# Performance work log

Measured on AMD Instinct MI355X. Metric: run time of the kernel, lower is better.

## Reference

```python
import jax, jax.numpy as jnp
import numpy as np

H = 8  # num_heads


def _ln(x, g, b):
    mu = x.mean(-1, keepdims=True)
    var = ((x - mu) ** 2).mean(-1, keepdims=True)
    return (x - mu) * jax.lax.rsqrt(var + 1e-5) * g + b


def setup_inputs() -> dict:
    key = jax.random.key(0)
    ks = jax.random.split(key, 24)
    B, N, V, E, D, R, L = 8, 512, 50000, 300, 256, 100, 4
    dh = D // H
    s = 0.02
    inp = {}
    inp['token_ids'] = jax.random.randint(ks[0], (B, N), 0, V, dtype=jnp.int32)
    inp['relations'] = jax.random.randint(ks[1], (B, N, N), 0, R, dtype=jnp.int32)
    m = jax.random.bernoulli(ks[2], 0.9, (B, N, N))
    eye = jnp.eye(N, dtype=bool)[None]
    inp['relations_mask'] = jnp.logical_or(m, eye)  # keep diagonal valid so every row attends somewhere
    inp['embed'] = jax.random.normal(ks[3], (V, E), jnp.float32) * s
    inp['W_in'] = jax.random.normal(ks[4], (E, D), jnp.float32) * s
    inp['b_in'] = jnp.zeros((D,), jnp.float32)
    inp['Wq'] = jax.random.normal(ks[5], (L, D, D), jnp.float32) * s
    inp['Wk'] = jax.random.normal(ks[6], (L, D, D), jnp.float32) * s
    inp['Wv'] = jax.random.normal(ks[7], (L, D, D), jnp.float32) * s
    inp['Wo'] = jax.random.normal(ks[8], (L, D, D), jnp.float32) * s
    inp['ln1_g'] = jnp.ones((L, D), jnp.float32)
    inp['ln1_b'] = jnp.zeros((L, D), jnp.float32)
    inp['ln2_g'] = jnp.ones((L, D), jnp.float32)
    inp['ln2_b'] = jnp.zeros((L, D), jnp.float32)
    inp['W1'] = jax.random.normal(ks[9], (L, D, 4 * D), jnp.float32) * s
    inp['b1'] = jnp.zeros((L, 4 * D), jnp.float32)
    inp['W2'] = jax.random.normal(ks[10], (L, 4 * D, D), jnp.float32) * s
    inp['b2'] = jnp.zeros((L, D), jnp.float32)
    inp['rel_k_emb'] = jax.random.normal(ks[11], (R, dh), jnp.float32) * s
    inp['rel_v_emb'] = jax.random.normal(ks[12], (R, dh), jnp.float32) * s
    inp['W_out'] = jax.random.normal(ks[13], (D, D), jnp.float32) * s
    inp['b_out'] = jnp.zeros((D,), jnp.float32)
    return inp


def reference(token_ids, relations, relations_mask, embed, W_in, b_in, Wq, Wk, Wv, Wo,
              ln1_g, ln1_b, ln2_g, ln2_b, W1, b1, W2, b2, rel_k_emb, rel_v_emb, W_out, b_out):
    # Input layer: embedding lookup + projection to gnn hidden size.
    x = embed[token_ids]                          # [B,N,E]
    x = jax.nn.relu(x @ W_in + b_in)              # [B,N,D]
    B, N, D = x.shape
    dh = D // H
    # Shared relation embeddings (share_layers=True, share_heads=True): gathered once.
    rk = rel_k_emb[relations]                     # [B,N,N,dh]
    rv = rel_v_emb[relations]                     # [B,N,N,dh]
    neg = jnp.asarray(-1e9, x.dtype)
    scale = jnp.asarray(1.0 / np.sqrt(dh), x.dtype)
    L = Wq.shape[0]
    for l in range(L):  # fixed small layer count
        q = (x @ Wq[l]).reshape(B, N, H, dh).transpose(0, 2, 1, 3)
        k = (x @ Wk[l]).reshape(B, N, H, dh).transpose(0, 2, 1, 3)
        v = (x @ Wv[l]).reshape(B, N, H, dh).transpose(0, 2, 1, 3)
        # Relation-aware scores: q.k + q.r_k (RAT-SQL)
        scores = (jnp.einsum('bhnd,bhmd->bhnm', q, k)
                  + jnp.einsum('bhnd,bnmd->bhnm', q, rk)) * scale
        scores = jnp.where(relations_mask[:, None], scores, neg)
        a = jax.nn.softmax(scores, axis=-1)       # [B,H,N,N]
        z = (jnp.einsum('bhnm,bhmd->bhnd', a, v)
             + jnp.einsum('bhnm,bnmd->bhnd', a, rv))
        z = z.transpose(0, 2, 1, 3).reshape(B, N, D) @ Wo[l]
        x = _ln(x + z, ln1_g[l], ln1_b[l])
        f = jax.nn.relu(x @ W1[l] + b1[l]) @ W2[l] + b2[l]
        x = _ln(x + f, ln2_g[l], ln2_b[l])
    # Output layer projection
    return x @ W_out + b_out
```

## Files before the change

### kernel.cpp

```cpp
#include <hip/hip_runtime.h>
#include <hip/hip_bf16.h>

#define NTOK 4096
#define NN   512

typedef __attribute__((ext_vector_type(8))) short bf16x8;
typedef __attribute__((ext_vector_type(4))) short bf16x4;
typedef __attribute__((ext_vector_type(4))) float f32x4;

__device__ __forceinline__ float bf16_to_f(unsigned short u) {
    unsigned int x = ((unsigned int)u) << 16;
    return __builtin_bit_cast(float, x);
}
__device__ __forceinline__ unsigned short f_to_bf16(float f) {
    unsigned int b = __builtin_bit_cast(unsigned int, f);
    return (unsigned short)((b + 0x7fff + ((b >> 16) & 1)) >> 16);
}
__device__ __forceinline__ bf16x8 pack8(float4 a, float4 b) {
    bf16x8 v;
    v[0]=(short)f_to_bf16(a.x); v[1]=(short)f_to_bf16(a.y);
    v[2]=(short)f_to_bf16(a.z); v[3]=(short)f_to_bf16(a.w);
    v[4]=(short)f_to_bf16(b.x); v[5]=(short)f_to_bf16(b.y);
    v[6]=(short)f_to_bf16(b.z); v[7]=(short)f_to_bf16(b.w);
    return v;
}

__global__ void detect_mask_kernel(const unsigned char* __restrict__ m, int* __restrict__ flag) {
    __shared__ int f;
    if (threadIdx.x == 0) f = 0;
    __syncthreads();
    int any = 0;
    for (int i = threadIdx.x; i < 4096; i += 256) {
        if ((i & 3) != 0 && m[i] != 0) any = 1;
    }
    if (any) atomicOr(&f, 1);
    __syncthreads();
    if (threadIdx.x == 0) *flag = f;
}

__global__ __launch_bounds__(256) void prep_rel16(
    const int* __restrict__ rel, const void* __restrict__ mask,
    const int* __restrict__ flag, short* __restrict__ rel16)
{
    const bool mbyte = (*flag != 0);
    const unsigned char* m8 = (const unsigned char*)mask;
    const int* m32 = (const int*)mask;
    const int i = (blockIdx.x * 256 + threadIdx.x) * 2;
    int2 rv = *(const int2*)(rel + i);
    int ok0, ok1;
    if (mbyte) { ok0 = m8[i]; ok1 = m8[i + 1]; }
    else       { ok0 = (m32[i] != 0); ok1 = (m32[i + 1] != 0); }
    short2 o;
    o.x = ok0 ? (short)rv.x : (short)-1;
    o.y = ok1 ? (short)rv.y : (short)-1;
    *(short2*)(rel16 + i) = o;
}

__global__ __launch_bounds__(256) void embed_proj_kernel(
    const int* __restrict__ tok, const float* __restrict__ embed,
    const float* __restrict__ W_in, const float* __restrict__ b_in,
    float* __restrict__ x)
{
    __shared__ float emb[8][304];
    __shared__ int tloc[8];
    const int t = threadIdx.x;
    const int r0 = blockIdx.x * 8;
    if (t < 8) tloc[t] = tok[r0 + t];
    __syncthreads();
    for (int i = t; i < 8 * 300; i += 256) {
        int r = i / 300, e = i - r * 300;
        emb[r][e] = embed[(size_t)tloc[r] * 300 + e];
    }
    __syncthreads();
    float acc[8] = {0.f,0.f,0.f,0.f,0.f,0.f,0.f,0.f};
    const int d = t;
    for (int e = 0; e < 300; ++e) {
        float w = W_in[e * 256 + d];
#pragma unroll
        for (int r = 0; r < 8; ++r) acc[r] += emb[r][e] * w;
    }
    const float bb = b_in[d];
#pragma unroll
    for (int r = 0; r < 8; ++r) {
        float o = acc[r] + bb;
        o = o > 0.f ? o : 0.f;
        x[(size_t)(r0 + r) * 256 + d] = o;
    }
}

__global__ __launch_bounds__(256) void gemm_mfma(
    const float* __restrict__ A,
    const float* __restrict__ W0, const float* __restrict__ W1p, const float* __restrict__ W2p,
    int ncPerW, const float* __restrict__ bias,
    float* __restrict__ C, int M, int K, int Nc, int relu)
{
    __shared__ unsigned short As[2][64][40];
    __shared__ unsigned short Bs[2][64][40];

    const int t = threadIdx.x;
    const int lane = t & 63, w = t >> 6;
    const int g = lane >> 4, li = lane & 15;
    const int r0 = blockIdx.y * 64, c0 = blockIdx.x * 64;

    const float* Wp = W0; int cW = c0;
    if (c0 >= 2 * ncPerW)      { Wp = W2p; cW = c0 - 2 * ncPerW; }
    else if (c0 >= ncPerW)     { Wp = W1p; cW = c0 - ncPerW; }

    f32x4 acc[4];
#pragma unroll
    for (int i = 0; i < 4; ++i) acc[i] = (f32x4){0.f, 0.f, 0.f, 0.f};

    const int arow = t >> 2, ad8 = (t & 3) * 8;
    const int bnn = t & 63, bk8 = (t >> 6) * 8;

    const float* ap0 = A + (size_t)(r0 + arow) * K + ad8;
    float4 a0 = *(const float4*)ap0;
    float4 a1 = *(const float4*)(ap0 + 4);
    float wv[8];
#pragma unroll
    for (int j = 0; j < 8; ++j)
        wv[j] = Wp[(size_t)(bk8 + j) * ncPerW + cW + bnn];

    const int nk = K >> 5;
    for (int ki = 0; ki < nk; ++ki) {
        const int cur = ki & 1;
        *(bf16x8*)&As[cur][arow][ad8] = pack8(a0, a1);
        {
            bf16x8 v;
#pragma unroll
            for (int j = 0; j < 8; ++j) v[j] = (short)f_to_bf16(wv[j]);
            *(bf16x8*)&Bs[cur][bnn][bk8] = v;
        }
        if (ki + 1 < nk) {
            const int k0 = (ki + 1) * 32;
            const float* ap = A + (size_t)(r0 + arow) * K + k0 + ad8;
            a0 = *(const float4*)ap;
            a1 = *(const float4*)(ap + 4);
#pragma unroll
            for (int j = 0; j < 8; ++j)
                wv[j] = Wp[(size_t)(k0 + bk8 + j) * ncPerW + cW + bnn];
        }
        __syncthreads();
        bf16x8 af = *(const bf16x8*)&As[cur][16 * w + li][g * 8];
#pragma unroll
        for (int sub = 0; sub < 4; ++sub) {
            bf16x8 bfr = *(const bf16x8*)&Bs[cur][16 * sub + li][g * 8];
            acc[sub] = __builtin_amdgcn_mfma_f32_16x16x32_bf16(af, bfr, acc[sub], 0, 0, 0);
        }
    }
#pragma unroll
    for (int sub = 0; sub < 4; ++sub) {
        int col = c0 + sub * 16 + li;
        float bv = bias ? bias[col] : 0.f;
#pragma unroll
        for (int r = 0; r < 4; ++r) {
            int row = r0 + 16 * w + g * 4 + r;
            float o = acc[sub][r] + bv;
            if (relu) o = fmaxf(o, 0.f);
            C[(size_t)row * Nc + col] = o;
        }
    }
}

__global__ __launch_bounds__(256) void gemm_mfma_128(
    const float* __restrict__ A,
    const float* __restrict__ W0, const float* __restrict__ W1p, const float* __restrict__ W2p,
    int ncPerW, const float* __restrict__ bias,
    float* __restrict__ C, int M, int K, int Nc, int relu)
{
    __shared__ unsigned short As[2][128][40];
    __shared__ unsigned short Bs[2][64][40];

    const int t = threadIdx.x;
    const int lane = t & 63, w = t >> 6;
    const int g = lane >> 4, li = lane & 15;
    const int r0 = blockIdx.y * 128, c0 = blockIdx.x * 64;

    const float* Wp = W0; int cW = c0;
    if (c0 >= 2 * ncPerW)      { Wp = W2p; cW = c0 - 2 * ncPerW; }
    else if (c0 >= ncPerW)     { Wp = W1p; cW = c0 - ncPerW; }

    f32x4 acc[2][4];
#pragma unroll
    for (int i = 0; i < 2; ++i)
#pragma unroll
        for (int j = 0; j < 4; ++j) acc[i][j] = (f32x4){0.f, 0.f, 0.f, 0.f};

    const int arow = t >> 1, ah = (t & 1) * 16;
    const int bnn = t & 63, bk8 = (t >> 6) * 8;

    const float* ap0 = A + (size_t)(r0 + arow) * K + ah;
    float4 a0 = *(const float4*)ap0;
    float4 a1 = *(const float4*)(ap0 + 4);
    float4 a2 = *(const float4*)(ap0 + 8);
    float4 a3 = *(const float4*)(ap0 + 12);
    float wv[8];
#pragma unroll
    for (int j = 0; j < 8; ++j)
        wv[j] = Wp[(size_t)(bk8 + j) * ncPerW + cW + bnn];

    const int nk = K >> 5;
    for (int ki = 0; ki < nk; ++ki) {
        const int cur = ki & 1;
        *(bf16x8*)&As[cur][arow][ah]     = pack8(a0, a1);
        *(bf16x8*)&As[cur][arow][ah + 8] = pack8(a2, a3);
        {
            bf16x8 v;
#pragma unroll
            for (int j = 0; j < 8; ++j) v[j] = (short)f_to_bf16(wv[j]);
            *(bf16x8*)&Bs[cur][bnn][bk8] = v;
        }
        if (ki + 1 < nk) {
            const int k0 = (ki + 1) * 32;
            const float* ap = A + (size_t)(r0 + arow) * K + k0 + ah;
            a0 = *(const float4*)ap;
            a1 = *(const float4*)(ap + 4);
            a2 = *(const float4*)(ap + 8);
            a3 = *(const float4*)(ap + 12);
#pragma unroll
            for (int j = 0; j < 8; ++j)
                wv[j] = Wp[(size_t)(k0 + bk8 + j) * ncPerW + cW + bnn];
        }
        __syncthreads();
        bf16x8 af0 = *(const bf16x8*)&As[cur][32 * w + li][g * 8];
        bf16x8 af1 = *(const bf16x8*)&As[cur][32 * w + 16 + li][g * 8];
#pragma unroll
        for (int sub = 0; sub < 4; ++sub) {
            bf16x8 bfr = *(const bf16x8*)&Bs[cur][16 * sub + li][g * 8];
            acc[0][sub] = __builtin_amdgcn_mfma_f32_16x16x32_bf16(af0, bfr, acc[0][sub], 0, 0, 0);
            acc[1][sub] = __builtin_amdgcn_mfma_f32_16x16x32_bf16(af1, bfr, acc[1][sub], 0, 0, 0);
        }
    }
#pragma unroll
    for (int rc = 0; rc < 2; ++rc)
#pragma unroll
    for (int sub = 0; sub < 4; ++sub) {
        int col = c0 + sub * 16 + li;
        float bv = bias ? bias[col] : 0.f;
#pragma unroll
        for (int r = 0; r < 4; ++r) {
            int row = r0 + 32 * w + rc * 16 + g * 4 + r;
            float o = acc[rc][sub][r] + bv;
            if (relu) o = fmaxf(o, 0.f);
            C[(size_t)row * Nc + col] = o;
        }
    }
}

__global__ __launch_bounds__(256) void qrk_kernel(
    const float* __restrict__ qkv, const float* __restrict__ relk_g,
    unsigned short* __restrict__ qrkg)
{
    const int n0 = blockIdx.x * 64, h = blockIdx.y, b = blockIdx.z;
    const int t = threadIdx.x, lane = t & 63, w = t >> 6;
    const int g = lane >> 4, li = lane & 15;
    const int qrow = 16 * w + g * 4;

    __shared__ unsigned short relk_s[100][40];
    for (int i = t; i < 400; i += 256) {
        int rr = i >> 2, d8 = (i & 3) * 8;
        const float* sp = relk_g + rr * 32 + d8;
        *(bf16x8*)&relk_s[rr][d8] = pack8(*(const float4*)sp, *(const float4*)(sp + 4));
    }
    const float scale = 0.17677669529663687f;
    bf16x8 qf;
    {
        const float* qp = qkv + (size_t)(b * NN + n0 + 16 * w + li) * 768 + h * 32 + g * 8;
        float4 q0 = *(const float4*)qp, q1 = *(const float4*)(qp + 4);
        q0.x *= scale; q0.y *= scale; q0.z *= scale; q0.w *= scale;
        q1.x *= scale; q1.y *= scale; q1.z *= scale; q1.w *= scale;
        qf = pack8(q0, q1);
    }
    __syncthreads();
#pragma unroll
    for (int rc = 0; rc < 7; ++rc) {
        bf16x8 bb = *(const bf16x8*)&relk_s[rc * 16 + li][g * 8];
        f32x4 s = __builtin_amdgcn_mfma_f32_16x16x32_bf16(qf, bb, (f32x4){0.f,0.f,0.f,0.f}, 0, 0, 0);
        int col = rc * 16 + li;
        if (col < 100) {
#pragma unroll
            for (int r = 0; r < 4; ++r)
                qrkg[((size_t)(b * 8 + h) * NN + n0 + qrow + r) * 100 + col] = f_to_bf16(s[r]);
        }
    }
}

__global__ __launch_bounds__(256, 4) void attn_mfma(
    const float* __restrict__ qkv,
    const short* __restrict__ rel16,
    const unsigned short* __restrict__ qrkg,
    const float* __restrict__ relv_g,
    float* __restrict__ zpart,
    float* __restrict__ smpart)
{
    const int p = blockIdx.x;
    const int cx = p & 7, idx0 = p >> 3;
    const int sg = cx * 8 + (idx0 >> 4);
    const int hm = idx0 & 15;
    const int h = hm >> 1, ms = hm & 1;
    const int b = sg >> 3, chunk = sg & 7;
    const int n0 = chunk * 64, mbase = ms * 256;

    const int t = threadIdx.x;
    const int lane = t & 63, w = t >> 6;
    const int g = lane >> 4, li = lane & 15;
    const int qrow = 16 * w + g * 4;

    __shared__ float wrel[64][100];
    __shared__ union {
        unsigned short relvT[32][136];
        struct {
            unsigned short v_t[2][32][40];
            unsigned short p_s[4][16][40];
        } mn;
    } u;

    for (int i = t; i < 6400; i += 256) ((float*)wrel)[i] = 0.f;
    const float scale = 0.17677669529663687f;
    bf16x8 qf;
    {
        const float* qp = qkv + (size_t)(b * NN + n0 + 16 * w + li) * 768 + h * 32 + g * 8;
        float4 q0 = *(const float4*)qp, q1 = *(const float4*)(qp + 4);
        q0.x *= scale; q0.y *= scale; q0.z *= scale; q0.w *= scale;
        q1.x *= scale; q1.y *= scale; q1.z *= scale; q1.w *= scale;
        qf = pack8(q0, q1);
    }
    const short* relrow[4];
    const unsigned short* qgr[4];
#pragma unroll
    for (int r = 0; r < 4; ++r) {
        relrow[r] = rel16 + ((size_t)b * NN + n0 + qrow + r) * NN;
        qgr[r] = qrkg + ((size_t)(b * 8 + h) * NN + n0 + qrow + r) * 100;
    }
    const int vm = t & 31, vdg = t >> 5;
    const size_t kRB = (size_t)(b * NN) * 768 + 256 + h * 32 + g * 8;
    const size_t vRB = (size_t)(b * NN) * 768 + 512 + h * 32 + vdg * 4;

    float4 kbuf[2][4]; float4 vbuf[2];
    short rbuf[2][8]; unsigned short qvb[2][8];
    {
#pragma unroll
        for (int i = 0; i < 8; ++i)
            rbuf[0][i] = relrow[i & 3][mbase + (i >> 2) * 16 + li];
        kbuf[0][0] = *(const float4*)(qkv + kRB + (size_t)(mbase + li) * 768);
        kbuf[0][1] = *(const float4*)(qkv + kRB + (size_t)(mbase + li) * 768 + 4);
        kbuf[0][2] = *(const float4*)(qkv + kRB + (size_t)(mbase + 16 + li) * 768);
        kbuf[0][3] = *(const float4*)(qkv + kRB + (size_t)(mbase + 16 + li) * 768 + 4);
        vbuf[0]    = *(const float4*)(qkv + vRB + (size_t)(mbase + vm) * 768);
#pragma unroll
        for (int i = 0; i < 8; ++i) {
            int rl = rbuf[0][i];
            qvb[0][i] = qgr[i & 3][rl < 0 ? 0 : rl];
        }
    }
    float smacc[4] = {0.f, 0.f, 0.f, 0.f};
    f32x4 zf[2];
    zf[0] = (f32x4){0.f,0.f,0.f,0.f};
    zf[1] = (f32x4){0.f,0.f,0.f,0.f};

    __syncthreads();

#pragma unroll
    for (int tt = 0; tt < 8; ++tt) {
        const int cur = tt & 1, nxt = cur ^ 1;
        {
            float4 vv = vbuf[cur];
            u.mn.v_t[cur][vdg * 4 + 0][vm] = f_to_bf16(vv.x);
            u.mn.v_t[cur][vdg * 4 + 1][vm] = f_to_bf16(vv.y);
            u.mn.v_t[cur][vdg * 4 + 2][vm] = f_to_bf16(vv.z);
            u.mn.v_t[cur][vdg * 4 + 3][vm] = f_to_bf16(vv.w);
        }
        if (tt + 1 < 8) {
            const int m0n = mbase + (tt + 1) * 32;
#pragma unroll
            for (int i = 0; i < 8; ++i)
                rbuf[nxt][i] = relrow[i & 3][m0n + (i >> 2) * 16 + li];
        }
        __syncthreads();
        bf16x8 kf0 = pack8(kbuf[cur][0], kbuf[cur][1]);
        bf16x8 kf1 = pack8(kbuf[cur][2], kbuf[cur][3]);
        if (tt + 1 < 8) {
            const int m0n = mbase + (tt + 1) * 32;
            kbuf[nxt][0] = *(const float4*)(qkv + kRB + (size_t)(m0n + li) * 768);
            kbuf[nxt][1] = *(const float4*)(qkv + kRB + (size_t)(m0n + li) * 768 + 4);
            kbuf[nxt][2] = *(const float4*)(qkv + kRB + (size_t)(m0n + 16 + li) * 768);
            kbuf[nxt][3] = *(const float4*)(qkv + kRB + (size_t)(m0n + 16 + li) * 768 + 4);
            vbuf[nxt]    = *(const float4*)(qkv + vRB + (size_t)(m0n + vm) * 768);
        }
        f32x4 s0 = __builtin_amdgcn_mfma_f32_16x16x32_bf16(qf, kf0, (f32x4){0.f,0.f,0.f,0.f}, 0, 0, 0);
        f32x4 s1 = __builtin_amdgcn_mfma_f32_16x16x32_bf16(qf, kf1, (f32x4){0.f,0.f,0.f,0.f}, 0, 0, 0);
        float pr[8];
#pragma unroll
        for (int i = 0; i < 8; ++i) {
            const int r = i & 3;
            const int rl = rbuf[cur][i];
            const float sv = ((i >> 2) ? s1[r] : s0[r]) + bf16_to_f(qvb[cur][i]);
            float pv = 0.f;
            if (rl >= 0) {
                pv = __expf(fminf(sv, 50.f));
                atomicAdd(&wrel[qrow + r][rl], pv);
            }
            smacc[r] += pv;
            pr[i] = pv;
        }
#pragma unroll
        for (int i = 0; i < 8; ++i)
            u.mn.p_s[w][g * 4 + (i & 3)][(i >> 2) * 16 + li] = f_to_bf16(pr[i]);
        if (tt + 1 < 8) {
#pragma unroll
            for (int i = 0; i < 8; ++i) {
                int rl = rbuf[nxt][i];
                qvb[nxt][i] = qgr[i & 3][rl < 0 ? 0 : rl];
            }
        }
        asm volatile("s_waitcnt lgkmcnt(0)" ::: "memory");
        __builtin_amdgcn_sched_barrier(0);
        bf16x8 pa = *(const bf16x8*)&u.mn.p_s[w][li][g * 8];
#pragma unroll
        for (int dc = 0; dc < 2; ++dc) {
            bf16x8 vb = *(const bf16x8*)&u.mn.v_t[cur][dc * 16 + li][g * 8];
            zf[dc] = __builtin_amdgcn_mfma_f32_16x16x32_bf16(pa, vb, zf[dc], 0, 0, 0);
        }
    }
    __syncthreads();

    for (int i = t; i < 32 * 36; i += 256) {
        int d = i / 36, c = 100 + (i - (i / 36) * 36);
        u.relvT[d][c] = 0;
    }
    for (int i = t; i < 400; i += 256) {
        int rr2 = i >> 2, d8 = (i & 3) * 8;
        const float* sp = relv_g + rr2 * 32 + d8;
        float4 s0 = *(const float4*)sp, s1 = *(const float4*)(sp + 4);
        u.relvT[d8 + 0][rr2] = f_to_bf16(s0.x);
        u.relvT[d8 + 1][rr2] = f_to_bf16(s0.y);
        u.relvT[d8 + 2][rr2] = f_to_bf16(s0.z);
        u.relvT[d8 + 3][rr2] = f_to_bf16(s0.w);
        u.relvT[d8 + 4][rr2] = f_to_bf16(s1.x);
        u.relvT[d8 + 5][rr2] = f_to_bf16(s1.y);
        u.relvT[d8 + 6][rr2] = f_to_bf16(s1.z);
        u.relvT[d8 + 7][rr2] = f_to_bf16(s1.w);
    }
    __syncthreads();

#pragma unroll
    for (int kc = 0; kc < 4; ++kc) {
        const int kbase = kc * 32 + g * 8;
        const float* wp = &wrel[16 * w + li][0];
        bf16x8 af;
#pragma unroll
        for (int j = 0; j < 8; ++j) {
            int id = kbase + j;
            float val = (id < 100) ? wp[id] : 0.f;
            af[j] = (short)f_to_bf16(val);
        }
#pragma unroll
        for (int dc = 0; dc < 2; ++dc) {
            bf16x8 vb = *(const bf16x8*)&u.relvT[dc * 16 + li][kbase];
            zf[dc] = __builtin_amdgcn_mfma_f32_16x16x32_bf16(af, vb, zf[dc], 0, 0, 0);
        }
    }

#pragma unroll
    for (int r = 0; r < 4; ++r) {
        smacc[r] += __shfl_xor(smacc[r], 1, 64);
        smacc[r] += __shfl_xor(smacc[r], 2, 64);
        smacc[r] += __shfl_xor(smacc[r], 4, 64);
        smacc[r] += __shfl_xor(smacc[r], 8, 64);
    }
#pragma unroll
    for (int r = 0; r < 4; ++r) {
        const int row = b * NN + n0 + qrow + r;
        size_t ob = (size_t)ms * 1048576 + (size_t)row * 256 + h * 32;
#pragma unroll
        for (int dc = 0; dc < 2; ++dc)
            zpart[ob + dc * 16 + li] = zf[dc][r];
        if (li == 0)
            smpart[(size_t)ms * 32768 + (size_t)row * 8 + h] = smacc[r];
    }
}

__global__ __launch_bounds__(256) void combine_kernel(
    const float* __restrict__ zpart, const float* __restrict__ smpart,
    float* __restrict__ z)
{
    const int t = threadIdx.x;
    const int wi = t >> 6, lane = t & 63;
    const int row = blockIdx.x * 4 + wi;
    const int h = lane >> 3;
    float den = 0.f;
    float4 acc = make_float4(0.f, 0.f, 0.f, 0.f);
#pragma unroll
    for (int s = 0; s < 2; ++s) {
        den += smpart[(size_t)s * 32768 + (size_t)row * 8 + h];
        float4 v = *(const float4*)(zpart + (size_t)s * 1048576 + (size_t)row * 256 + lane * 4);
        acc.x += v.x; acc.y += v.y; acc.z += v.z; acc.w += v.w;
    }
    const float inv = 1.f / den;
    acc.x *= inv; acc.y *= inv; acc.z *= inv; acc.w *= inv;
    *(float4*)(z + (size_t)row * 256 + lane * 4) = acc;
}

__global__ __launch_bounds__(256) void ln_kernel(
    const float* __restrict__ xin, const float* __restrict__ y,
    const float* __restrict__ g, const float* __restrict__ bsh,
    float* __restrict__ xout)
{
    const int t = threadIdx.x;
    const int w = t >> 6, lane = t & 63;
    const size_t row = (size_t)blockIdx.x * 4 + w;
    const float4 xv = *(const float4*)(xin + row * 256 + lane * 4);
    const float4 yv = *(const float4*)(y + row * 256 + lane * 4);
    float4 sv;
    sv.x = xv.x + yv.x; sv.y = xv.y + yv.y; sv.z = xv.z + yv.z; sv.w = xv.w + yv.w;
    float sum = sv.x + sv.y + sv.z + sv.w;
    float sq  = sv.x * sv.x + sv.y * sv.y + sv.z * sv.z + sv.w * sv.w;
#pragma unroll
    for (int off = 1; off < 64; off <<= 1) {
        sum += __shfl_xor(sum, off, 64);
        sq  += __shfl_xor(sq, off, 64);
    }
    const float mu = sum * (1.f / 256.f);
    const float var = sq * (1.f / 256.f) - mu * mu;
    const float rs = rsqrtf(var + 1e-5f);
    const float4 gv = *(const float4*)(g + lane * 4);
    const float4 bv = *(const float4*)(bsh + lane * 4);
    float4 o;
    o.x = (sv.x - mu) * rs * gv.x + bv.x;
    o.y = (sv.y - mu) * rs * gv.y + bv.y;
    o.z = (sv.z - mu) * rs * gv.z + bv.z;
    o.w = (sv.w - mu) * rs * gv.w + bv.w;
    *(float4*)(xout + row * 256 + lane * 4) = o;
}

extern "C" void kernel_launch(void* const* d_in, const int* in_sizes, int n_in,
                              void* d_out, int out_size, void* d_ws, size_t ws_size,
                              hipStream_t stream)
{
    (void)in_sizes; (void)n_in; (void)out_size;
    const int*   tok   = (const int*)d_in[0];
    const int*   rel   = (const int*)d_in[1];
    const void*  mask  = d_in[2];
    const float* embed = (const float*)d_in[3];
    const float* W_in  = (const float*)d_in[4];
    const float* b_in  = (const float*)d_in[5];
    const float* Wq    = (const float*)d_in[6];
    const float* Wk    = (const float*)d_in[7];
    const float* Wv    = (const float*)d_in[8];
    const float* Wo    = (const float*)d_in[9];
    const float* ln1g  = (const float*)d_in[10];
    const float* ln1b  = (const float*)d_in[11];
    const float* ln2g  = (const float*)d_in[12];
    const float* ln2b  = (const float*)d_in[13];
    const float* W1    = (const float*)d_in[14];
    const float* b1    = (const float*)d_in[15];
    const float* W2    = (const float*)d_in[16];
    const float* b2    = (const float*)d_in[17];
    const float* relk  = (const float*)d_in[18];
    const float* relv  = (const float*)d_in[19];
    const float* Wout  = (const float*)d_in[20];
    const float* bout  = (const float*)d_in[21];
    float* out = (float*)d_out;

    float* ws  = (float*)d_ws;
    float* x   = ws;
    float* z   = ws + (1u << 20);
    float* zo  = ws + 2u * (1u << 20);
    float* qkv = ws + 3u * (1u << 20);
    float* hb  = ws + 6u * (1u << 20);

    const bool roomy = ws_size >= ((size_t)45 << 20);
    short* rel16 = roomy ? (short*)(ws + 10u * (1u << 20)) : (short*)z;
    int*   flag  = (int*)(ws + (roomy ? 11u : 10u) * (1u << 20));
    float* zpart = hb;
    unsigned short* qrkg = (unsigned short*)(hb + 2u * (1u << 20));
    float* smpart = zo;

    detect_mask_kernel<<<1, 256, 0, stream>>>((const unsigned char*)mask, flag);
    if (roomy)
        prep_rel16<<<4096, 256, 0, stream>>>(rel, mask, flag, rel16);
    embed_proj_kernel<<<512, 256, 0, stream>>>(tok, embed, W_in, b_in, x);

    for (int l = 0; l < 4; ++l) {
        const float* wq = Wq + (size_t)l * 65536;
        const float* wk = Wk + (size_t)l * 65536;
        const float* wv = Wv + (size_t)l * 65536;
        const float* wo = Wo + (size_t)l * 65536;
        const float* w1 = W1 + (size_t)l * 262144;
        const float* w2 = W2 + (size_t)l * 262144;

        if (!roomy)
            prep_rel16<<<4096, 256, 0, stream>>>(rel, mask, flag, rel16);

        gemm_mfma_128<<<dim3(12, 32), 256, 0, stream>>>(x, wq, wk, wv, 256, nullptr,
                                                        qkv, NTOK, 256, 768, 0);
        qrk_kernel<<<dim3(8, 8, 8), 256, 0, stream>>>(qkv, relk, qrkg);
        attn_mfma<<<1024, 256, 0, stream>>>(qkv, rel16, qrkg, relv, zpart, smpart);
        combine_kernel<<<1024, 256, 0, stream>>>(zpart, smpart, z);
        gemm_mfma<<<dim3(4, 64), 256, 0, stream>>>(z, wo, wo, wo, 256, nullptr,
                                                   zo, NTOK, 256, 256, 0);
        ln_kernel<<<1024, 256, 0, stream>>>(x, zo, ln1g + l * 256, ln1b + l * 256, x);
        gemm_mfma_128<<<dim3(16, 32), 256, 0, stream>>>(x, w1, w1, w1, 1024, b1 + l * 1024,
                                                        hb, NTOK, 256, 1024, 1);
        gemm_mfma<<<dim3(4, 64), 256, 0, stream>>>(hb, w2, w2, w2, 256, b2 + l * 256,
                                                   zo, NTOK, 1024, 256, 0);
        ln_kernel<<<1024, 256, 0, stream>>>(x, zo, ln2g + l * 256, ln2b + l * 256, x);
    }
    gemm_mfma<<<dim3(4, 64), 256, 0, stream>>>(x, Wout, Wout, Wout, 256, bout,
                                               out, NTOK, 256, 256, 0);
}
```

Before: 705.9 us.

## Keep activations and pre-transposed weights in bf16 across GEMMs and attention

Weights are transposed and cast to bf16 once at the start, with the attention scale folded into Wq. Activations (x, qkv, z, FFN hidden) are now produced directly in bf16 by the GEMM epilogues, layernorm and combine kernels, so later kernels load half the bytes and skip the per-tile float-to-bf16 packing. The attention kernel also stages the per-row relation-key scores in LDS instead of gathering them from global memory, and lowers its occupancy hint from 4 to 3. In exchange there are extra upfront cast kernels, more workspace, and slightly different rounding on the hidden activations.

Measured after the change: 646.8 us. 1.09x faster.

```diff
diff --git a/kernel.cpp b/kernel.cpp
--- a/kernel.cpp
+++ b/kernel.cpp
@@ -5,8 +5,8 @@
 #define NN   512
 
 typedef __attribute__((ext_vector_type(8))) short bf16x8;
-typedef __attribute__((ext_vector_type(4))) short bf16x4;
 typedef __attribute__((ext_vector_type(4))) float f32x4;
+typedef __attribute__((ext_vector_type(4))) unsigned short u16x4;
 
 __device__ __forceinline__ float bf16_to_f(unsigned short u) {
     unsigned int x = ((unsigned int)u) << 16;
@@ -56,10 +56,58 @@
     *(short2*)(rel16 + i) = o;
 }
 
+__global__ __launch_bounds__(256) void tcast256(
+    const float* __restrict__ Wq, const float* __restrict__ Wk,
+    const float* __restrict__ Wv, const float* __restrict__ Wo,
+    const float* __restrict__ Wout, unsigned short* __restrict__ wt,
+    int nL, float scale)
+{
+    const int z = blockIdx.z;
+    const float* src; unsigned short* dst; float sc = 1.f;
+    if (z >= nL * 4) {
+        src = Wout; dst = wt + (size_t)nL * 786432;
+    } else {
+        const int l = z >> 2, which = z & 3;
+        if      (which == 0) { src = Wq + (size_t)l * 65536; sc = scale; }
+        else if (which == 1) { src = Wk + (size_t)l * 65536; }
+        else if (which == 2) { src = Wv + (size_t)l * 65536; }
+        else                 { src = Wo + (size_t)l * 65536; }
+        dst = wt + (size_t)l * 786432 + which * 65536;
+    }
+    __shared__ float tile[32][33];
+    const int t = threadIdx.x, tx = t & 31, ty = t >> 5;
+    const int n0 = blockIdx.x * 32, k0 = blockIdx.y * 32;
+#pragma unroll
+    for (int p = 0; p < 4; ++p)
+        tile[ty + p * 8][tx] = src[(size_t)(k0 + ty + p * 8) * 256 + n0 + tx];
+    __syncthreads();
+#pragma unroll
+    for (int p = 0; p < 4; ++p)
+        dst[(size_t)(n0 + ty + p * 8) * 256 + k0 + tx] = f_to_bf16(tile[tx][ty + p * 8] * sc);
+}
+
+__global__ __launch_bounds__(256) void tcastKN(
+    const float* __restrict__ in, unsigned short* __restrict__ out,
+    int K, int N, long inStride, long outStride)
+{
+    in  += (size_t)blockIdx.z * inStride;
+    out += (size_t)blockIdx.z * outStride;
+    __shared__ float tile[32][33];
+    const int t = threadIdx.x, tx = t & 31, ty = t >> 5;
+    const int n0 = blockIdx.x * 32, k0 = blockIdx.y * 32;
+#pragma unroll
+    for (int p = 0; p < 4; ++p)
+        tile[ty + p * 8][tx] = in[(size_t)(k0 + ty + p * 8) * N + n0 + tx];
+    __syncthreads();
+#pragma unroll
+    for (int p = 0; p < 4; ++p)
+        out[(size_t)(n0 + ty + p * 8) * K + k0 + tx] = f_to_bf16(tile[tx][ty + p * 8]);
+}
+
 __global__ __launch_bounds__(256) void embed_proj_kernel(
     const int* __restrict__ tok, const float* __restrict__ embed,
     const float* __restrict__ W_in, const float* __restrict__ b_in,
-    float* __restrict__ x)
+    float* __restrict__ x, unsigned short* __restrict__ xh)
 {
     __shared__ float emb[8][304];
     __shared__ int tloc[8];
@@ -85,60 +133,40 @@
         float o = acc[r] + bb;
         o = o > 0.f ? o : 0.f;
         x[(size_t)(r0 + r) * 256 + d] = o;
-    }
-}
-
-__global__ __launch_bounds__(256) void gemm_mfma(
-    const float* __restrict__ A,
-    const float* __restrict__ W0, const float* __restrict__ W1p, const float* __restrict__ W2p,
-    int ncPerW, const float* __restrict__ bias,
-    float* __restrict__ C, int M, int K, int Nc, int relu)
+        xh[(size_t)(r0 + r) * 256 + d] = f_to_bf16(o);
+    }
+}
+
+__global__ __launch_bounds__(256) void gemm_bf16_64(
+    const unsigned short* __restrict__ A, const unsigned short* __restrict__ WT,
+    const float* __restrict__ bias, float* __restrict__ Cf, unsigned short* __restrict__ Ch,
+    int M, int K, int Nc, int relu)
 {
     __shared__ unsigned short As[2][64][40];
     __shared__ unsigned short Bs[2][64][40];
-
     const int t = threadIdx.x;
     const int lane = t & 63, w = t >> 6;
     const int g = lane >> 4, li = lane & 15;
     const int r0 = blockIdx.y * 64, c0 = blockIdx.x * 64;
 
-    const float* Wp = W0; int cW = c0;
-    if (c0 >= 2 * ncPerW)      { Wp = W2p; cW = c0 - 2 * ncPerW; }
-    else if (c0 >= ncPerW)     { Wp = W1p; cW = c0 - ncPerW; }
-
     f32x4 acc[4];
 #pragma unroll
-    for (int i = 0; i < 4; ++i) acc[i] = (f32x4){0.f, 0.f, 0.f, 0.f};
+    for (int i = 0; i < 4; ++i) acc[i] = (f32x4){0.f,0.f,0.f,0.f};
 
     const int arow = t >> 2, ad8 = (t & 3) * 8;
-    const int bnn = t & 63, bk8 = (t >> 6) * 8;
-
-    const float* ap0 = A + (size_t)(r0 + arow) * K + ad8;
-    float4 a0 = *(const float4*)ap0;
-    float4 a1 = *(const float4*)(ap0 + 4);
-    float wv[8];
-#pragma unroll
-    for (int j = 0; j < 8; ++j)
-        wv[j] = Wp[(size_t)(bk8 + j) * ncPerW + cW + bnn];
+
+    bf16x8 a0 = *(const bf16x8*)(A  + (size_t)(r0 + arow) * K + ad8);
+    bf16x8 b0 = *(const bf16x8*)(WT + (size_t)(c0 + arow) * K + ad8);
 
     const int nk = K >> 5;
     for (int ki = 0; ki < nk; ++ki) {
         const int cur = ki & 1;
-        *(bf16x8*)&As[cur][arow][ad8] = pack8(a0, a1);
-        {
-            bf16x8 v;
-#pragma unroll
-            for (int j = 0; j < 8; ++j) v[j] = (short)f_to_bf16(wv[j]);
-            *(bf16x8*)&Bs[cur][bnn][bk8] = v;
-        }
+        *(bf16x8*)&As[cur][arow][ad8] = a0;
+        *(bf16x8*)&Bs[cur][arow][ad8] = b0;
         if (ki + 1 < nk) {
             const int k0 = (ki + 1) * 32;
-            const float* ap = A + (size_t)(r0 + arow) * K + k0 + ad8;
-            a0 = *(const float4*)ap;
-            a1 = *(const float4*)(ap + 4);
-#pragma unroll
-            for (int j = 0; j < 8; ++j)
-                wv[j] = Wp[(size_t)(k0 + bk8 + j) * ncPerW + cW + bnn];
+            a0 = *(const bf16x8*)(A  + (size_t)(r0 + arow) * K + k0 + ad8);
+            b0 = *(const bf16x8*)(WT + (size_t)(c0 + arow) * K + k0 + ad8);
         }
         __syncthreads();
         bf16x8 af = *(const bf16x8*)&As[cur][16 * w + li][g * 8];
@@ -157,69 +185,48 @@
             int row = r0 + 16 * w + g * 4 + r;
             float o = acc[sub][r] + bv;
             if (relu) o = fmaxf(o, 0.f);
-            C[(size_t)row * Nc + col] = o;
-        }
-    }
-}
-
-__global__ __launch_bounds__(256) void gemm_mfma_128(
-    const float* __restrict__ A,
-    const float* __restrict__ W0, const float* __restrict__ W1p, const float* __restrict__ W2p,
-    int ncPerW, const float* __restrict__ bias,
-    float* __restrict__ C, int M, int K, int Nc, int relu)
+            if (Ch) Ch[(size_t)row * Nc + col] = f_to_bf16(o);
+            else    Cf[(size_t)row * Nc + col] = o;
+        }
+    }
+}
+
+__global__ __launch_bounds__(256) void gemm_bf16_128(
+    const unsigned short* __restrict__ A, const unsigned short* __restrict__ WT,
+    const float* __restrict__ bias, float* __restrict__ Cf, unsigned short* __restrict__ Ch,
+    int M, int K, int Nc, int relu)
 {
     __shared__ unsigned short As[2][128][40];
     __shared__ unsigned short Bs[2][64][40];
-
     const int t = threadIdx.x;
     const int lane = t & 63, w = t >> 6;
     const int g = lane >> 4, li = lane & 15;
     const int r0 = blockIdx.y * 128, c0 = blockIdx.x * 64;
 
-    const float* Wp = W0; int cW = c0;
-    if (c0 >= 2 * ncPerW)      { Wp = W2p; cW = c0 - 2 * ncPerW; }
-    else if (c0 >= ncPerW)     { Wp = W1p; cW = c0 - ncPerW; }
-
     f32x4 acc[2][4];
 #pragma unroll
     for (int i = 0; i < 2; ++i)
 #pragma unroll
-        for (int j = 0; j < 4; ++j) acc[i][j] = (f32x4){0.f, 0.f, 0.f, 0.f};
+        for (int j = 0; j < 4; ++j) acc[i][j] = (f32x4){0.f,0.f,0.f,0.f};
 
     const int arow = t >> 1, ah = (t & 1) * 16;
-    const int bnn = t & 63, bk8 = (t >> 6) * 8;
-
-    const float* ap0 = A + (size_t)(r0 + arow) * K + ah;
-    float4 a0 = *(const float4*)ap0;
-    float4 a1 = *(const float4*)(ap0 + 4);
-    float4 a2 = *(const float4*)(ap0 + 8);
-    float4 a3 = *(const float4*)(ap0 + 12);
-    float wv[8];
-#pragma unroll
-    for (int j = 0; j < 8; ++j)
-        wv[j] = Wp[(size_t)(bk8 + j) * ncPerW + cW + bnn];
+    const int bcol = t >> 2, bk8 = (t & 3) * 8;
+
+    bf16x8 a0 = *(const bf16x8*)(A + (size_t)(r0 + arow) * K + ah);
+    bf16x8 a1 = *(const bf16x8*)(A + (size_t)(r0 + arow) * K + ah + 8);
+    bf16x8 b0 = *(const bf16x8*)(WT + (size_t)(c0 + bcol) * K + bk8);
 
     const int nk = K >> 5;
     for (int ki = 0; ki < nk; ++ki) {
         const int cur = ki & 1;
-        *(bf16x8*)&As[cur][arow][ah]     = pack8(a0, a1);
-        *(bf16x8*)&As[cur][arow][ah + 8] = pack8(a2, a3);
-        {
-            bf16x8 v;
-#pragma unroll
-            for (int j = 0; j < 8; ++j) v[j] = (short)f_to_bf16(wv[j]);
-            *(bf16x8*)&Bs[cur][bnn][bk8] = v;
-        }
+        *(bf16x8*)&As[cur][arow][ah]     = a0;
+        *(bf16x8*)&As[cur][arow][ah + 8] = a1;
+        *(bf16x8*)&Bs[cur][bcol][bk8]    = b0;
         if (ki + 1 < nk) {
             const int k0 = (ki + 1) * 32;
-            const float* ap = A + (size_t)(r0 + arow) * K + k0 + ah;
-            a0 = *(const float4*)ap;
-            a1 = *(const float4*)(ap + 4);
-            a2 = *(const float4*)(ap + 8);
-            a3 = *(const float4*)(ap + 12);
-#pragma unroll
-            for (int j = 0; j < 8; ++j)
-                wv[j] = Wp[(size_t)(k0 + bk8 + j) * ncPerW + cW + bnn];
+            a0 = *(const bf16x8*)(A + (size_t)(r0 + arow) * K + k0 + ah);
+            a1 = *(const bf16x8*)(A + (size_t)(r0 + arow) * K + k0 + ah + 8);
+            b0 = *(const bf16x8*)(WT + (size_t)(c0 + bcol) * K + k0 + bk8);
         }
         __syncthreads();
         bf16x8 af0 = *(const bf16x8*)&As[cur][32 * w + li][g * 8];
@@ -242,13 +249,14 @@
             int row = r0 + 32 * w + rc * 16 + g * 4 + r;
             float o = acc[rc][sub][r] + bv;
             if (relu) o = fmaxf(o, 0.f);
-            C[(size_t)row * Nc + col] = o;
+            if (Ch) Ch[(size_t)row * Nc + col] = f_to_bf16(o);
+            else    Cf[(size_t)row * Nc + col] = o;
         }
     }
 }
 
 __global__ __launch_bounds__(256) void qrk_kernel(
-    const float* __restrict__ qkv, const float* __restrict__ relk_g,
+    const unsigned short* __restrict__ qkvh, const float* __restrict__ relk_g,
     unsigned short* __restrict__ qrkg)
 {
     const int n0 = blockIdx.x * 64, h = blockIdx.y, b = blockIdx.z;
@@ -262,15 +270,7 @@
         const float* sp = relk_g + rr * 32 + d8;
         *(bf16x8*)&relk_s[rr][d8] = pack8(*(const float4*)sp, *(const float4*)(sp + 4));
     }
-    const float scale = 0.17677669529663687f;
-    bf16x8 qf;
-    {
-        const float* qp = qkv + (size_t)(b * NN + n0 + 16 * w + li) * 768 + h * 32 + g * 8;
-        float4 q0 = *(const float4*)qp, q1 = *(const float4*)(qp + 4);
-        q0.x *= scale; q0.y *= scale; q0.z *= scale; q0.w *= scale;
-        q1.x *= scale; q1.y *= scale; q1.z *= scale; q1.w *= scale;
-        qf = pack8(q0, q1);
-    }
+    bf16x8 qf = *(const bf16x8*)(qkvh + (size_t)(b * NN + n0 + 16 * w + li) * 768 + h * 32 + g * 8);
     __syncthreads();
 #pragma unroll
     for (int rc = 0; rc < 7; ++rc) {
@@ -285,13 +285,12 @@
     }
 }
 
-__global__ __launch_bounds__(256, 4) void attn_mfma(
-    const float* __restrict__ qkv,
+__global__ __launch_bounds__(256, 3) void attn_mfma(
+    const unsigned short* __restrict__ qkvh,
     const short* __restrict__ rel16,
     const unsigned short* __restrict__ qrkg,
     const float* __restrict__ relv_g,
-    float* __restrict__ zpart,
-    float* __restrict__ smpart)
+    float* __restrict__ zpart, float* __restrict__ smpart)
 {
     const int p = blockIdx.x;
     const int cx = p & 7, idx0 = p >> 3;
@@ -307,6 +306,7 @@
     const int qrow = 16 * w + g * 4;
 
     __shared__ float wrel[64][100];
+    __shared__ unsigned short qrk_lds[64][100];
     __shared__ union {
         unsigned short relvT[32][136];
         struct {
@@ -316,43 +316,32 @@
     } u;
 
     for (int i = t; i < 6400; i += 256) ((float*)wrel)[i] = 0.f;
-    const float scale = 0.17677669529663687f;
-    bf16x8 qf;
     {
-        const float* qp = qkv + (size_t)(b * NN + n0 + 16 * w + li) * 768 + h * 32 + g * 8;
-        float4 q0 = *(const float4*)qp, q1 = *(const float4*)(qp + 4);
-        q0.x *= scale; q0.y *= scale; q0.z *= scale; q0.w *= scale;
-        q1.x *= scale; q1.y *= scale; q1.z *= scale; q1.w *= scale;
-        qf = pack8(q0, q1);
-    }
+        const unsigned short* qsrc = qrkg + ((size_t)(b * 8 + h) * NN + n0) * 100;
+        for (int i = t; i < 3200; i += 256) {
+            int row = i / 50, off = (i - row * 50) * 2;
+            *(unsigned int*)&qrk_lds[row][off] =
+                *(const unsigned int*)(qsrc + (size_t)row * 100 + off);
+        }
+    }
+    bf16x8 qf = *(const bf16x8*)(qkvh + (size_t)(b * NN + n0 + 16 * w + li) * 768 + h * 32 + g * 8);
+
     const short* relrow[4];
-    const unsigned short* qgr[4];
-#pragma unroll
-    for (int r = 0; r < 4; ++r) {
+#pragma unroll
+    for (int r = 0; r < 4; ++r)
         relrow[r] = rel16 + ((size_t)b * NN + n0 + qrow + r) * NN;
-        qgr[r] = qrkg + ((size_t)(b * 8 + h) * NN + n0 + qrow + r) * 100;
-    }
     const int vm = t & 31, vdg = t >> 5;
     const size_t kRB = (size_t)(b * NN) * 768 + 256 + h * 32 + g * 8;
     const size_t vRB = (size_t)(b * NN) * 768 + 512 + h * 32 + vdg * 4;
 
-    float4 kbuf[2][4]; float4 vbuf[2];
-    short rbuf[2][8]; unsigned short qvb[2][8];
-    {
-#pragma unroll
-        for (int i = 0; i < 8; ++i)
-            rbuf[0][i] = relrow[i & 3][mbase + (i >> 2) * 16 + li];
-        kbuf[0][0] = *(const float4*)(qkv + kRB + (size_t)(mbase + li) * 768);
-        kbuf[0][1] = *(const float4*)(qkv + kRB + (size_t)(mbase + li) * 768 + 4);
-        kbuf[0][2] = *(const float4*)(qkv + kRB + (size_t)(mbase + 16 + li) * 768);
-        kbuf[0][3] = *(const float4*)(qkv + kRB + (size_t)(mbase + 16 + li) * 768 + 4);
-        vbuf[0]    = *(const float4*)(qkv + vRB + (size_t)(mbase + vm) * 768);
-#pragma unroll
-        for (int i = 0; i < 8; ++i) {
-            int rl = rbuf[0][i];
-            qvb[0][i] = qgr[i & 3][rl < 0 ? 0 : rl];
-        }
-    }
+    bf16x8 kbuf[2][2]; u16x4 vbuf[2]; short rbuf[2][8];
+#pragma unroll
+    for (int i = 0; i < 8; ++i)
+        rbuf[0][i] = relrow[i & 3][mbase + (i >> 2) * 16 + li];
+    kbuf[0][0] = *(const bf16x8*)(qkvh + kRB + (size_t)(mbase + li) * 768);
+    kbuf[0][1] = *(const bf16x8*)(qkvh + kRB + (size_t)(mbase + 16 + li) * 768);
+    vbuf[0]    = *(const u16x4*)(qkvh + vRB + (size_t)(mbase + vm) * 768);
+
     float smacc[4] = {0.f, 0.f, 0.f, 0.f};
     f32x4 zf[2];
     zf[0] = (f32x4){0.f,0.f,0.f,0.f};
@@ -363,13 +352,10 @@
 #pragma unroll
     for (int tt = 0; tt < 8; ++tt) {
         const int cur = tt & 1, nxt = cur ^ 1;
-        {
-            float4 vv = vbuf[cur];
-            u.mn.v_t[cur][vdg * 4 + 0][vm] = f_to_bf16(vv.x);
-            u.mn.v_t[cur][vdg * 4 + 1][vm] = f_to_bf16(vv.y);
-            u.mn.v_t[cur][vdg * 4 + 2][vm] = f_to_bf16(vv.z);
-            u.mn.v_t[cur][vdg * 4 + 3][vm] = f_to_bf16(vv.w);
-        }
+        u.mn.v_t[cur][vdg * 4 + 0][vm] = vbuf[cur][0];
+        u.mn.v_t[cur][vdg * 4 + 1][vm] = vbuf[cur][1];
+        u.mn.v_t[cur][vdg * 4 + 2][vm] = vbuf[cur][2];
+        u.mn.v_t[cur][vdg * 4 + 3][vm] = vbuf[cur][3];
         if (tt + 1 < 8) {
             const int m0n = mbase + (tt + 1) * 32;
 #pragma unroll
@@ -377,15 +363,12 @@
                 rbuf[nxt][i] = relrow[i & 3][m0n + (i >> 2) * 16 + li];
         }
         __syncthreads();
-        bf16x8 kf0 = pack8(kbuf[cur][0], kbuf[cur][1]);
-        bf16x8 kf1 = pack8(kbuf[cur][2], kbuf[cur][3]);
+        bf16x8 kf0 = kbuf[cur][0], kf1 = kbuf[cur][1];
         if (tt + 1 < 8) {
             const int m0n = mbase + (tt + 1) * 32;
-            kbuf[nxt][0] = *(const float4*)(qkv + kRB + (size_t)(m0n + li) * 768);
-            kbuf[nxt][1] = *(const float4*)(qkv + kRB + (size_t)(m0n + li) * 768 + 4);
-            kbuf[nxt][2] = *(const float4*)(qkv + kRB + (size_t)(m0n + 16 + li) * 768);
-            kbuf[nxt][3] = *(const float4*)(qkv + kRB + (size_t)(m0n + 16 + li) * 768 + 4);
-            vbuf[nxt]    = *(const float4*)(qkv + vRB + (size_t)(m0n + vm) * 768);
+            kbuf[nxt][0] = *(const bf16x8*)(qkvh + kRB + (size_t)(m0n + li) * 768);
+            kbuf[nxt][1] = *(const bf16x8*)(qkvh + kRB + (size_t)(m0n + 16 + li) * 768);
+            vbuf[nxt]    = *(const u16x4*)(qkvh + vRB + (size_t)(m0n + vm) * 768);
         }
         f32x4 s0 = __builtin_amdgcn_mfma_f32_16x16x32_bf16(qf, kf0, (f32x4){0.f,0.f,0.f,0.f}, 0, 0, 0);
         f32x4 s1 = __builtin_amdgcn_mfma_f32_16x16x32_bf16(qf, kf1, (f32x4){0.f,0.f,0.f,0.f}, 0, 0, 0);
@@ -394,7 +377,8 @@
         for (int i = 0; i < 8; ++i) {
             const int r = i & 3;
             const int rl = rbuf[cur][i];
-            const float sv = ((i >> 2) ? s1[r] : s0[r]) + bf16_to_f(qvb[cur][i]);
+            const float qadd = bf16_to_f(qrk_lds[qrow + r][rl < 0 ? 0 : rl]);
+            const float sv = ((i >> 2) ? s1[r] : s0[r]) + qadd;
             float pv = 0.f;
             if (rl >= 0) {
                 pv = __expf(fminf(sv, 50.f));
@@ -406,13 +390,6 @@
 #pragma unroll
         for (int i = 0; i < 8; ++i)
             u.mn.p_s[w][g * 4 + (i & 3)][(i >> 2) * 16 + li] = f_to_bf16(pr[i]);
-        if (tt + 1 < 8) {
-#pragma unroll
-            for (int i = 0; i < 8; ++i) {
-                int rl = rbuf[nxt][i];
-                qvb[nxt][i] = qgr[i & 3][rl < 0 ? 0 : rl];
-            }
-        }
         asm volatile("s_waitcnt lgkmcnt(0)" ::: "memory");
         __builtin_amdgcn_sched_barrier(0);
         bf16x8 pa = *(const bf16x8*)&u.mn.p_s[w][li][g * 8];
@@ -442,7 +419,6 @@
         u.relvT[d8 + 7][rr2] = f_to_bf16(s1.w);
     }
     __syncthreads();
-
 #pragma unroll
     for (int kc = 0; kc < 4; ++kc) {
         const int kbase = kc * 32 + g * 8;
@@ -460,7 +436,6 @@
             zf[dc] = __builtin_amdgcn_mfma_f32_16x16x32_bf16(af, vb, zf[dc], 0, 0, 0);
         }
     }
-
 #pragma unroll
     for (int r = 0; r < 4; ++r) {
         smacc[r] += __shfl_xor(smacc[r], 1, 64);
@@ -482,7 +457,7 @@
 
 __global__ __launch_bounds__(256) void combine_kernel(
     const float* __restrict__ zpart, const float* __restrict__ smpart,
-    float* __restrict__ z)
+    unsigned short* __restrict__ zbf)
 {
     const int t = threadIdx.x;
     const int wi = t >> 6, lane = t & 63;
@@ -497,14 +472,18 @@
         acc.x += v.x; acc.y += v.y; acc.z += v.z; acc.w += v.w;
     }
     const float inv = 1.f / den;
-    acc.x *= inv; acc.y *= inv; acc.z *= inv; acc.w *= inv;
-    *(float4*)(z + (size_t)row * 256 + lane * 4) = acc;
+    u16x4 oh;
+    oh[0] = f_to_bf16(acc.x * inv);
+    oh[1] = f_to_bf16(acc.y * inv);
+    oh[2] = f_to_bf16(acc.z * inv);
+    oh[3] = f_to_bf16(acc.w * inv);
+    *(u16x4*)(zbf + (size_t)row * 256 + lane * 4) = oh;
 }
 
 __global__ __launch_bounds__(256) void ln_kernel(
     const float* __restrict__ xin, const float* __restrict__ y,
     const float* __restrict__ g, const float* __restrict__ bsh,
-    float* __restrict__ xout)
+    float* __restrict__ xout, unsigned short* __restrict__ xh)
 {
     const int t = threadIdx.x;
     const int w = t >> 6, lane = t & 63;
@@ -531,6 +510,10 @@
     o.z = (sv.z - mu) * rs * gv.z + bv.z;
     o.w = (sv.w - mu) * rs * gv.w + bv.w;
     *(float4*)(xout + row * 256 + lane * 4) = o;
+    u16x4 oh;
+    oh[0] = f_to_bf16(o.x); oh[1] = f_to_bf16(o.y);
+    oh[2] = f_to_bf16(o.z); oh[3] = f_to_bf16(o.w);
+    *(u16x4*)(xh + row * 256 + lane * 4) = oh;
 }
 
 extern "C" void kernel_launch(void* const* d_in, const int* in_sizes, int n_in,
@@ -561,51 +544,64 @@
     const float* Wout  = (const float*)d_in[20];
     const float* bout  = (const float*)d_in[21];
     float* out = (float*)d_out;
-
-    float* ws  = (float*)d_ws;
-    float* x   = ws;
-    float* z   = ws + (1u << 20);
-    float* zo  = ws + 2u * (1u << 20);
-    float* qkv = ws + 3u * (1u << 20);
-    float* hb  = ws + 6u * (1u << 20);
-
-    const bool roomy = ws_size >= ((size_t)45 << 20);
-    short* rel16 = roomy ? (short*)(ws + 10u * (1u << 20)) : (short*)z;
-    int*   flag  = (int*)(ws + (roomy ? 11u : 10u) * (1u << 20));
-    float* zpart = hb;
-    unsigned short* qrkg = (unsigned short*)(hb + 2u * (1u << 20));
-    float* smpart = zo;
+    const float scale = 0.17677669529663687f;
+
+    float* ws = (float*)d_ws;
+    float*          x     = ws;
+    unsigned short* xh    = (unsigned short*)(ws + 1048576);
+    unsigned short* zbf   = (unsigned short*)(ws + 1572864);
+    float*          zo    = ws + 2097152;
+    unsigned short* qkvh  = (unsigned short*)(ws + 3145728);
+    unsigned short* hbh   = (unsigned short*)(ws + 4718592);
+    float*          zpart = ws + 6815744;
+    float*          smpart= ws + 8912896;
+    unsigned short* qrkg  = (unsigned short*)(ws + 8978432);
+    int*            flag  = (int*)(ws + 10616832);
+    unsigned short* wt    = (unsigned short*)(ws + 10616848);
+
+    const size_t wsf = ws_size >> 2;
+    const bool tierA = wsf >= 13271100;
+    short* rel16 = tierA ? (short*)(ws + 12222480) : (short*)hbh;
 
     detect_mask_kernel<<<1, 256, 0, stream>>>((const unsigned char*)mask, flag);
-    if (roomy)
+    embed_proj_kernel<<<512, 256, 0, stream>>>(tok, embed, W_in, b_in, x, xh);
+    if (tierA) {
         prep_rel16<<<4096, 256, 0, stream>>>(rel, mask, flag, rel16);
-    embed_proj_kernel<<<512, 256, 0, stream>>>(tok, embed, W_in, b_in, x);
+        tcast256<<<dim3(8, 8, 17), 256, 0, stream>>>(Wq, Wk, Wv, Wo, Wout, wt, 4, scale);
+        tcastKN<<<dim3(32, 8, 4), 256, 0, stream>>>(W1, wt + 262144, 256, 1024, 262144, 786432);
+        tcastKN<<<dim3(8, 32, 4), 256, 0, stream>>>(W2, wt + 524288, 1024, 256, 262144, 786432);
+    }
 
     for (int l = 0; l < 4; ++l) {
-        const float* wq = Wq + (size_t)l * 65536;
-        const float* wk = Wk + (size_t)l * 65536;
-        const float* wv = Wv + (size_t)l * 65536;
-        const float* wo = Wo + (size_t)l * 65536;
-        const float* w1 = W1 + (size_t)l * 262144;
-        const float* w2 = W2 + (size_t)l * 262144;
-
-        if (!roomy)
+        unsigned short* wl = tierA ? wt + (size_t)l * 786432 : wt;
+        if (!tierA) {
             prep_rel16<<<4096, 256, 0, stream>>>(rel, mask, flag, rel16);
-
-        gemm_mfma_128<<<dim3(12, 32), 256, 0, stream>>>(x, wq, wk, wv, 256, nullptr,
-                                                        qkv, NTOK, 256, 768, 0);
-        qrk_kernel<<<dim3(8, 8, 8), 256, 0, stream>>>(qkv, relk, qrkg);
-        attn_mfma<<<1024, 256, 0, stream>>>(qkv, rel16, qrkg, relv, zpart, smpart);
-        combine_kernel<<<1024, 256, 0, stream>>>(zpart, smpart, z);
-        gemm_mfma<<<dim3(4, 64), 256, 0, stream>>>(z, wo, wo, wo, 256, nullptr,
-                                                   zo, NTOK, 256, 256, 0);
-        ln_kernel<<<1024, 256, 0, stream>>>(x, zo, ln1g + l * 256, ln1b + l * 256, x);
-        gemm_mfma_128<<<dim3(16, 32), 256, 0, stream>>>(x, w1, w1, w1, 1024, b1 + l * 1024,
-                                                        hb, NTOK, 256, 1024, 1);
-        gemm_mfma<<<dim3(4, 64), 256, 0, stream>>>(hb, w2, w2, w2, 256, b2 + l * 256,
-                                                   zo, NTOK, 1024, 256, 0);
-        ln_kernel<<<1024, 256, 0, stream>>>(x, zo, ln2g + l * 256, ln2b + l * 256, x);
-    }
-    gemm_mfma<<<dim3(4, 64), 256, 0, stream>>>(x, Wout, Wout, Wout, 256, bout,
-                                               out, NTOK, 256, 256, 0);
-}
+            tcast256<<<dim3(8, 8, 4), 256, 0, stream>>>(
+                Wq + (size_t)l * 65536, Wk + (size_t)l * 65536,
+                Wv + (size_t)l * 65536, Wo + (size_t)l * 65536, Wout, wt, 1, scale);
+            tcastKN<<<dim3(32, 8, 1), 256, 0, stream>>>(W1 + (size_t)l * 262144, wt + 262144, 256, 1024, 0, 0);
+            tcastKN<<<dim3(8, 32, 1), 256, 0, stream>>>(W2 + (size_t)l * 262144, wt + 524288, 1024, 256, 0, 0);
+        }
+        gemm_bf16_128<<<dim3(12, 32), 256, 0, stream>>>(xh, wl, nullptr, nullptr, qkvh,
+                                                        NTOK, 256, 768, 0);
+        qrk_kernel<<<dim3(8, 8, 8), 256, 0, stream>>>(qkvh, relk, qrkg);
+        attn_mfma<<<1024, 256, 0, stream>>>(qkvh, rel16, qrkg, relv, zpart, smpart);
+        combine_kernel<<<1024, 256, 0, stream>>>(zpart, smpart, zbf);
+        gemm_bf16_64<<<dim3(4, 64), 256, 0, stream>>>(zbf, wl + 196608, nullptr, zo, nullptr,
+                                                      NTOK, 256, 256, 0);
+        ln_kernel<<<1024, 256, 0, stream>>>(x, zo, ln1g + l * 256, ln1b + l * 256, x, xh);
+        gemm_bf16_128<<<dim3(16, 32), 256, 0, stream>>>(xh, wl + 262144, b1 + l * 1024, nullptr, hbh,
+                                                        NTOK, 256, 1024, 1);
+        gemm_bf16_64<<<dim3(4, 64), 256, 0, stream>>>(hbh, wl + 524288, b2 + l * 256, zo, nullptr,
+                                                      NTOK, 1024, 256, 0);
+        ln_kernel<<<1024, 256, 0, stream>>>(x, zo, ln2g + l * 256, ln2b + l * 256, x, xh);
+    }
+    unsigned short* woutT = wt;
+    if (tierA) {
+        woutT = wt + (size_t)4 * 786432;
+    } else {
+        tcast256<<<dim3(8, 8, 1), 256, 0, stream>>>(Wq, Wk, Wv, Wo, Wout, wt, 0, scale);
+    }
+    gemm_bf16_64<<<dim3(4, 64), 256, 0, stream>>>(xh, woutT, bout, out, nullptr,
+                                                  NTOK, 256, 256, 0);
+}
```
